# Performance work log

Hardware: AMD Instinct MI355X
Metric: run time of the kernel (lower is better)

## Reference

```python
import jax, jax.numpy as jnp
import numpy as np
from jax.scipy.linalg import expm

N_LEAVES = 8   # n
S = 64         # alphabet size (codons)
M = 8          # number of mixture model components (prod(model_shape))
N_SITES = 100000
N_NODES = 15   # n leaves + k=7 internal nodes, root = node 14


def _build_tree():
    # T[child, parent] = branch length; balanced binary tree, children < parent
    T = np.zeros((N_NODES, N_NODES), dtype=np.float32)
    parent = [8, 8, 9, 9, 10, 10, 11, 11, 12, 12, 13, 13, 14, 14]
    for c, p in enumerate(parent):
        T[c, p] = 0.05 * (1 + (c % 4))
    return T

TREE = _build_tree()


def _inv_stereographic_projection(y):
    ns = jnp.sum(y * y, axis=-1, keepdims=True)          # (M, 1)
    return jnp.concatenate([2 * y, ns - 1], axis=-1) / (ns + 1)  # (M, s)


def _build_Q(rates, pi_inv):
    r = rates ** 2                                        # (M, s(s-1)/2), nonneg
    pi = _inv_stereographic_projection(pi_inv) ** 2       # (M, s) stable probs
    iu, ju = np.triu_indices(S, 1)
    Q = jnp.zeros((M, S, S), r.dtype).at[:, iu, ju].set(r)
    Q = Q + jnp.swapaxes(Q, 1, 2)                         # symmetrize (zero diag)
    Q = Q * pi[:, None, :]
    diag = -jnp.sum(Q, axis=2)                            # (M, s)
    Q = Q.at[:, jnp.arange(S), jnp.arange(S)].set(diag)
    emut = -jnp.sum(pi * diag, axis=1)                    # expected mutations
    Q = Q / emut[:, None, None]                           # one expected mutation
    return Q, pi


def _forward(X, rates, pi_inv):
    Q, pi = _build_Q(rates, pi_inv)
    es, et = np.nonzero(TREE)                             # static edge list
    n = N_LEAVES
    k = TREE.shape[-1] - n
    t = jnp.asarray(TREE[es, et])                         # (E,) branch lengths
    # all per-edge, per-component transition matrices: expm(t * Q)
    P = jax.vmap(expm)((t[:, None, None, None] * Q[None]).reshape(-1, S, S))
    P = P.reshape(len(es), M, S, S)                       # (E, M, s, s)
    A = []  # messages at internal nodes, each (i, M, s)
    for a in range(n, n + k):
        edge_ids = np.nonzero(et == a)[0]
        msgs = []
        for ei in edge_ids:
            b = int(es[ei])
            Pab = P[ei]                                   # (M, s, s)
            if b < n:
                msgs.append(jnp.einsum('mcd,id->imc', Pab, X[:, b, :]))
            else:
                msgs.append(jnp.einsum('mcd,imd->imc', Pab, A[b - n]))
        Aa = msgs[0]
        for mmsg in msgs[1:]:
            Aa = Aa * mmsg                                # Felsenstein product
        A.append(Aa)
    # marginalize root states against stationary distribution
    return jnp.einsum('imc,mc->im', A[-1], pi)            # (i, M)


def setup_inputs() -> dict:
    key = jax.random.key(0)
    k1, k2, k3 = jax.random.split(key, 3)
    X = jax.random.uniform(k1, (N_SITES, N_LEAVES, S), dtype=jnp.float32)
    rates = jax.random.uniform(k2, (M, S * (S - 1) // 2), dtype=jnp.float32)
    pi_inv = jax.random.uniform(k3, (M, S - 1), dtype=jnp.float32)
    return {'X': X, 'rates': rates, 'pi_inv': pi_inv}


def reference(X, rates, pi_inv):
    return _forward(X, rates, pi_inv)
```

## Files before the change

### kernel.cpp

```cpp
#include <hip/hip_runtime.h>

#define NS 100000

typedef _Float16 half8v __attribute__((ext_vector_type(8)));
typedef _Float16 half4v __attribute__((ext_vector_type(4)));
typedef _Float16 half2v __attribute__((ext_vector_type(2)));
typedef float    f32x16 __attribute__((ext_vector_type(16)));
typedef unsigned int uint2v __attribute__((ext_vector_type(2)));

__device__ __forceinline__ float wave_sum64(float v) {
#pragma unroll
  for (int off = 32; off > 0; off >>= 1) v += __shfl_xor(v, off, 64);
  return v;
}
__device__ __forceinline__ float wave_max64(float v) {
#pragma unroll
  for (int off = 32; off > 0; off >>= 1) v = fmaxf(v, __shfl_xor(v, off, 64));
  return v;
}

__device__ __forceinline__ void mm64(const float* __restrict__ Lt,
                                     const float* __restrict__ Rn,
                                     int ro, int co, float r[16]) {
#pragma unroll 4
  for (int kk0 = 0; kk0 < 64; kk0 += 4) {
    float4 tv[4], av[4];
#pragma unroll
    for (int j = 0; j < 4; ++j) {
      tv[j] = *(const float4*)(Lt + (kk0 + j) * 64 + ro);
      av[j] = *(const float4*)(Rn + (kk0 + j) * 64 + co);
    }
#pragma unroll
    for (int j = 0; j < 4; ++j) {
      const float* tp = (const float*)&tv[j];
      const float* ap = (const float*)&av[j];
#pragma unroll
      for (int i = 0; i < 4; ++i)
#pragma unroll
        for (int c = 0; c < 4; ++c) r[i * 4 + c] += tp[i] * ap[c];
    }
  }
}

__global__ __launch_bounds__(256) void prep_P(const float* __restrict__ rates,
                                              const float* __restrict__ pi_inv,
                                              _Float16* __restrict__ Pw) {
  __shared__ __align__(16) float Ab[4096];
  __shared__ __align__(16) float Tt[4096];
  __shared__ __align__(16) float Sb[4096];
  __shared__ float pi_l[64];
  __shared__ float sc_sh[2];
  const int t = threadIdx.x;
  const int m = blockIdx.x;

  if (t < 64) {
    float y = (t < 63) ? pi_inv[m * 63 + t] : 0.f;
    float ns = wave_sum64(y * y);
    float ps = (t < 63) ? (2.f * y / (ns + 1.f)) : ((ns - 1.f) / (ns + 1.f));
    pi_l[t] = ps * ps;
  }
  __syncthreads();

  for (int it = 0; it < 16; ++it) {
    int e = t + 256 * it, i = e >> 6, j = e & 63;
    float v = 0.f;
    if (i != j) {
      int ii = i < j ? i : j, jj = i < j ? j : i;
      int tri = ii * 63 - (ii * (ii - 1)) / 2 + (jj - ii - 1);
      float r = rates[m * 2016 + tri];
      v = r * r * pi_l[j];
    }
    Ab[e] = v;
  }
  __syncthreads();
  if (t < 64) {
    float s = 0.f;
    for (int j = 0; j < 64; ++j) s += Ab[t * 64 + ((j + t) & 63)];
    Ab[t * 64 + t] = -s;
    float em = wave_sum64(pi_l[t] * s);
    if (t == 0) sc_sh[0] = 0.05f / em;
  }
  __syncthreads();
  const float sc0 = sc_sh[0];
  if (t < 64) {
    float s = 0.f;
    for (int i = 0; i < 64; ++i) s += fabsf(Ab[i * 64 + t]);
    float n1 = wave_max64(s * fabsf(sc0));
    if (t == 0) {
      int sq = 0;
      while (n1 > 0.25f && sq < 24) { n1 *= 0.5f; ++sq; }
      sc_sh[0] = ldexpf(sc0, -sq);
      sc_sh[1] = (float)sq;
    }
  }
  __syncthreads();
  const float scl = sc_sh[0];
  const int   sq  = (int)sc_sh[1];
  for (int it = 0; it < 16; ++it) {
    int e = t + 256 * it, i = e >> 6, j = e & 63;
    float a = Ab[e] * scl;
    Ab[e] = a;
    Tt[j * 64 + i] = a;
  }
  __syncthreads();

  const int ro = (t >> 4) * 4, co = (t & 15) * 4;
  float ss[16];
#pragma unroll
  for (int i = 0; i < 16; ++i) ss[i] = 0.f;

  for (int k = 2; k <= 8; ++k) {
    float r[16];
#pragma unroll
    for (int i = 0; i < 16; ++i) r[i] = 0.f;
    mm64(Tt, Ab, ro, co, r);
    __syncthreads();
    float inv = 1.f / (float)k;
#pragma unroll
    for (int i = 0; i < 16; ++i) { r[i] *= inv; ss[i] += r[i]; }
#pragma unroll
    for (int j = 0; j < 4; ++j) {
      float4 w = {r[0 * 4 + j], r[1 * 4 + j], r[2 * 4 + j], r[3 * 4 + j]};
      *(float4*)(Tt + (co + j) * 64 + ro) = w;
    }
    __syncthreads();
  }

  float s[16];
#pragma unroll
  for (int i = 0; i < 4; ++i)
#pragma unroll
    for (int j = 0; j < 4; ++j)
      s[i * 4 + j] = ss[i * 4 + j] + Ab[(ro + i) * 64 + co + j] +
                     (((ro + i) == (co + j)) ? 1.f : 0.f);
  __syncthreads();
#pragma unroll
  for (int i = 0; i < 4; ++i) {
    float4 w = {s[i * 4 + 0], s[i * 4 + 1], s[i * 4 + 2], s[i * 4 + 3]};
    *(float4*)(Sb + (ro + i) * 64 + co) = w;
  }
#pragma unroll
  for (int j = 0; j < 4; ++j) {
    float4 w = {s[0 * 4 + j], s[1 * 4 + j], s[2 * 4 + j], s[3 * 4 + j]};
    *(float4*)(Tt + (co + j) * 64 + ro) = w;
  }
  __syncthreads();

  for (int q = 0; q < sq; ++q) {
    float r[16];
#pragma unroll
    for (int i = 0; i < 16; ++i) r[i] = 0.f;
    mm64(Tt, Sb, ro, co, r);
    __syncthreads();
#pragma unroll
    for (int i = 0; i < 16; ++i) s[i] = r[i];
#pragma unroll
    for (int i = 0; i < 4; ++i) {
      float4 w = {s[i * 4 + 0], s[i * 4 + 1], s[i * 4 + 2], s[i * 4 + 3]};
      *(float4*)(Sb + (ro + i) * 64 + co) = w;
    }
#pragma unroll
    for (int j = 0; j < 4; ++j) {
      float4 w = {s[0 * 4 + j], s[1 * 4 + j], s[2 * 4 + j], s[3 * 4 + j]};
      *(float4*)(Tt + (co + j) * 64 + ro) = w;
    }
    __syncthreads();
  }

  _Float16* base = Pw + (size_t)m * 5 * 4096;
#pragma unroll
  for (int i = 0; i < 4; ++i) {
    half4v h1, h4;
#pragma unroll
    for (int j = 0; j < 4; ++j) {
      float v = s[i * 4 + j];
      h1[j] = (_Float16)v;
      h4[j] = (_Float16)(pi_l[ro + i] * v);
    }
    *(half4v*)(base + (ro + i) * 64 + co)            = h1;
    *(half4v*)(base + 4 * 4096 + (ro + i) * 64 + co) = h4;
  }
  float p2[16];
#pragma unroll
  for (int i = 0; i < 16; ++i) p2[i] = 0.f;
  mm64(Tt, Sb, ro, co, p2);
  __syncthreads();
#pragma unroll
  for (int i = 0; i < 4; ++i) {
    float4 w = {p2[i * 4 + 0], p2[i * 4 + 1], p2[i * 4 + 2], p2[i * 4 + 3]};
    *(float4*)(Ab + (ro + i) * 64 + co) = w;
    half4v h;
#pragma unroll
    for (int j = 0; j < 4; ++j) h[j] = (_Float16)p2[i * 4 + j];
    *(half4v*)(base + 1 * 4096 + (ro + i) * 64 + co) = h;
  }
#pragma unroll
  for (int j = 0; j < 4; ++j) {
    float4 w = {p2[0 * 4 + j], p2[1 * 4 + j], p2[2 * 4 + j], p2[3 * 4 + j]};
    *(float4*)(Tt + (co + j) * 64 + ro) = w;
  }
  __syncthreads();
  {
    float r3[16], r4[16];
#pragma unroll
    for (int i = 0; i < 16; ++i) { r3[i] = 0.f; r4[i] = 0.f; }
#pragma unroll 2
    for (int kk0 = 0; kk0 < 64; kk0 += 4) {
      float4 tv[4], a3[4], a4[4];
#pragma unroll
      for (int j = 0; j < 4; ++j) {
        tv[j] = *(const float4*)(Tt + (kk0 + j) * 64 + ro);
        a3[j] = *(const float4*)(Sb + (kk0 + j) * 64 + co);
        a4[j] = *(const float4*)(Ab + (kk0 + j) * 64 + co);
      }
#pragma unroll
      for (int j = 0; j < 4; ++j) {
        const float* tp = (const float*)&tv[j];
        const float* p3 = (const float*)&a3[j];
        const float* p4 = (const float*)&a4[j];
#pragma unroll
        for (int i = 0; i < 4; ++i)
#pragma unroll
          for (int c = 0; c < 4; ++c) {
            r3[i * 4 + c] += tp[i] * p3[c];
            r4[i * 4 + c] += tp[i] * p4[c];
          }
      }
    }
#pragma unroll
    for (int i = 0; i < 4; ++i) {
      half4v h3, h4;
#pragma unroll
      for (int j = 0; j < 4; ++j) {
        h3[j] = (_Float16)r3[i * 4 + j];
        h4[j] = (_Float16)r4[i * 4 + j];
      }
      *(half4v*)(base + 2 * 4096 + (ro + i) * 64 + co) = h3;
      *(half4v*)(base + 3 * 4096 + (ro + i) * 64 + co) = h4;
    }
  }
}

struct Pk { half2v h[16]; };
struct PF { half8v f0[4], f1[4]; };

__device__ __forceinline__ void swap32(unsigned& a, unsigned& b) {
#if __has_builtin(__builtin_amdgcn_permlane32_swap)
  uint2v r = __builtin_amdgcn_permlane32_swap(a, b, false, false);
  a = r.x; b = r.y;
#else
  unsigned pa = (unsigned)__shfl_xor((int)a, 32, 64);
  unsigned pb = (unsigned)__shfl_xor((int)b, 32, 64);
  bool hi = (threadIdx.x & 32) != 0;
  unsigned na = hi ? pb : a;
  unsigned nb = hi ? b : pa;
  a = na; b = nb;
#endif
}

__device__ __forceinline__ half8v bfrag_state(const Pk& s, int kt) {
  const int rt = kt >> 1, b = (kt & 1) * 4;
  unsigned a0 = __builtin_bit_cast(unsigned, s.h[rt * 8 + b + 0]);
  unsigned c0 = __builtin_bit_cast(unsigned, s.h[rt * 8 + b + 2]);
  unsigned a1 = __builtin_bit_cast(unsigned, s.h[rt * 8 + b + 1]);
  unsigned c1 = __builtin_bit_cast(unsigned, s.h[rt * 8 + b + 3]);
  swap32(a0, c0);
  swap32(a1, c1);
  union { half8v v; unsigned u[4]; } U;
  U.u[0] = a0; U.u[1] = a1; U.u[2] = c0; U.u[3] = c1;
  return U.v;
}

__device__ __forceinline__ void zero16(f32x16& a) {
#pragma unroll
  for (int i = 0; i < 16; ++i) a[i] = 0.f;
}

__device__ __forceinline__ Pk pack_acc(const f32x16& a0, const f32x16& a1) {
  Pk o;
#pragma unroll
  for (int p = 0; p < 8; ++p) {
    o.h[p]     = __builtin_bit_cast(half2v,
                   __builtin_amdgcn_cvt_pkrtz(a0[2 * p], a0[2 * p + 1]));
    o.h[8 + p] = __builtin_bit_cast(half2v,
                   __builtin_amdgcn_cvt_pkrtz(a1[2 * p], a1[2 * p + 1]));
  }
  return o;
}

__device__ __forceinline__ PF load_pf(const _Float16* __restrict__ Pv,
                                      int s31, int hb) {
  PF pf;
#pragma unroll
  for (int kt = 0; kt < 4; ++kt) {
    pf.f0[kt] = *(const half8v*)(Pv + (s31 * 64 + kt * 16 + hb * 8));
    pf.f1[kt] = *(const half8v*)(Pv + ((32 + s31) * 64 + kt * 16 + hb * 8));
  }
  return pf;
}

__device__ __forceinline__ Pk msg_leaf_pk(const _Float16* __restrict__ Pv,
                                          const _Float16* __restrict__ xs,
                                          int leaf, int s31, int hb, int sw) {
  PF pf = load_pf(Pv, s31, hb);
  f32x16 a0, a1;
  zero16(a0); zero16(a1);
#pragma unroll
  for (int kt = 0; kt < 4; ++kt) {
    half8v bf = *(const half8v*)(xs + s31 * 512 +
                                 ((leaf * 64 + kt * 16 + hb * 8) ^ sw));
    a0 = __builtin_amdgcn_mfma_f32_32x32x16_f16(pf.f0[kt], bf, a0, 0, 0, 0);
    a1 = __builtin_amdgcn_mfma_f32_32x32x16_f16(pf.f1[kt], bf, a1, 0, 0, 0);
  }
  return pack_acc(a0, a1);
}

__device__ __forceinline__ Pk msg_state_pk(const _Float16* __restrict__ Pv,
                                           const Pk& src, int s31, int hb) {
  PF pf = load_pf(Pv, s31, hb);
  f32x16 a0, a1;
  zero16(a0); zero16(a1);
#pragma unroll
  for (int kt = 0; kt < 4; ++kt) {
    half8v bf = bfrag_state(src, kt);
    a0 = __builtin_amdgcn_mfma_f32_32x32x16_f16(pf.f0[kt], bf, a0, 0, 0, 0);
    a1 = __builtin_amdgcn_mfma_f32_32x32x16_f16(pf.f1[kt], bf, a1, 0, 0, 0);
  }
  return pack_acc(a0, a1);
}

__device__ __forceinline__ Pk mulpk(const Pk& a, const Pk& b) {
  Pk o;
#pragma unroll
  for (int i = 0; i < 16; ++i) o.h[i] = a.h[i] * b.h[i];
  return o;
}

__global__ __launch_bounds__(256, 2) void tree_fwd(const float* __restrict__ X,
                                                   const _Float16* __restrict__ Pw,
                                                   float* __restrict__ out) {
  __shared__ __align__(16) _Float16 xs[32 * 512];
  const int t = threadIdx.x;
  const int sb0 = blockIdx.x * 32;

  for (int it = 0; it < 16; ++it) {
    int e0 = (t + 256 * it) * 4;
    int site = e0 >> 9;
    int k = e0 & 511;
    float4 v = ((const float4*)X)[(size_t)(sb0 + site) * 128 + (k >> 2)];
    half4v h;
    h.x = (_Float16)v.x; h.y = (_Float16)v.y; h.z = (_Float16)v.z; h.w = (_Float16)v.w;
    *(half4v*)(xs + site * 512 + (k ^ ((site & 7) << 3))) = h;
  }
  __syncthreads();

  const int lane = t & 63, wav = t >> 6;
  const int s31 = lane & 31, hb = lane >> 5;
  const int sw = (s31 & 7) << 3;

#pragma unroll 1
  for (int mp = 0; mp < 2; ++mp) {
    const int m = wav + 4 * mp;
    const _Float16* Pm = Pw + (size_t)m * 5 * 4096;

    Pk sA = mulpk(msg_leaf_pk(Pm + 0 * 4096, xs, 0, s31, hb, sw),
                  msg_leaf_pk(Pm + 1 * 4096, xs, 1, s31, hb, sw));
    Pk sB = mulpk(msg_leaf_pk(Pm + 2 * 4096, xs, 2, s31, hb, sw),
                  msg_leaf_pk(Pm + 3 * 4096, xs, 3, s31, hb, sw));
    Pk s12 = mulpk(msg_state_pk(Pm + 0 * 4096, sA, s31, hb),
                   msg_state_pk(Pm + 1 * 4096, sB, s31, hb));
    sA = mulpk(msg_leaf_pk(Pm + 0 * 4096, xs, 4, s31, hb, sw),
               msg_leaf_pk(Pm + 1 * 4096, xs, 5, s31, hb, sw));
    sB = mulpk(msg_leaf_pk(Pm + 2 * 4096, xs, 6, s31, hb, sw),
               msg_leaf_pk(Pm + 3 * 4096, xs, 7, s31, hb, sw));
    Pk s13 = mulpk(msg_state_pk(Pm + 2 * 4096, sA, s31, hb),
                   msg_state_pk(Pm + 3 * 4096, sB, s31, hb));
    Pk mL = msg_state_pk(Pm + 4 * 4096, s12, s31, hb);
    {
      PF pf = load_pf(Pm + 1 * 4096, s31, hb);
      f32x16 a0, a1;
      zero16(a0); zero16(a1);
#pragma unroll
      for (int kt = 0; kt < 4; ++kt) {
        half8v bf = bfrag_state(s13, kt);
        a0 = __builtin_amdgcn_mfma_f32_32x32x16_f16(pf.f0[kt], bf, a0, 0, 0, 0);
        a1 = __builtin_amdgcn_mfma_f32_32x32x16_f16(pf.f1[kt], bf, a1, 0, 0, 0);
      }
      float part = 0.f;
#pragma unroll
      for (int p = 0; p < 8; ++p) {
        part += (float)mL.h[p].x     * a0[2 * p]
              + (float)mL.h[p].y     * a0[2 * p + 1]
              + (float)mL.h[8 + p].x * a1[2 * p]
              + (float)mL.h[8 + p].y * a1[2 * p + 1];
      }
      part += __shfl_xor(part, 32, 64);
      if (lane < 32) out[(size_t)(sb0 + s31) * 8 + m] = part;
    }
  }
}

extern "C" void kernel_launch(void* const* d_in, const int* in_sizes, int n_in,
                              void* d_out, int out_size, void* d_ws, size_t ws_size,
                              hipStream_t stream) {
  const float* X      = (const float*)d_in[0];
  const float* rates  = (const float*)d_in[1];
  const float* pi_inv = (const float*)d_in[2];
  _Float16* Pw = (_Float16*)d_ws;

  prep_P<<<8, 256, 0, stream>>>(rates, pi_inv, Pw);
  tree_fwd<<<NS / 32, 256, 0, stream>>>(X, Pw, (float*)d_out);
}
```

Before: 523.9 us.

## Use 64-site blocks, split waves by site group and component, reuse P fragments

Each block now handles 64 sites instead of 32. The four waves are split into two site groups, and each wave covers four mixture components instead of two. Leaf messages are computed in pairs that share one loaded set of P fragments, and the accumulators are processed one 32-row half at a time, which lowers register pressure and the number of global loads of P. The Taylor series in prep_P is cut from 8 terms to 6, which trades expm accuracy for less setup work. LDS use doubles to 64 KB per block, which may limit occupancy, and a bounds guard is added for the partial last block.

Result: slower. 567.4 us (+8.3%).

```diff
diff --git a/kernel.cpp b/kernel.cpp
--- a/kernel.cpp
+++ b/kernel.cpp
@@ -109,7 +109,7 @@
 #pragma unroll
   for (int i = 0; i < 16; ++i) ss[i] = 0.f;
 
-  for (int k = 2; k <= 8; ++k) {
+  for (int k = 2; k <= 6; ++k) {
     float r[16];
 #pragma unroll
     for (int i = 0; i < 16; ++i) r[i] = 0.f;
@@ -242,7 +242,6 @@
 }
 
 struct Pk { half2v h[16]; };
-struct PF { half8v f0[4], f1[4]; };
 
 __device__ __forceinline__ void swap32(unsigned& a, unsigned& b) {
 #if __has_builtin(__builtin_amdgcn_permlane32_swap)
@@ -276,57 +275,90 @@
   for (int i = 0; i < 16; ++i) a[i] = 0.f;
 }
 
-__device__ __forceinline__ Pk pack_acc(const f32x16& a0, const f32x16& a1) {
+__device__ __forceinline__ half2v pk2(float x, float y) {
+  half2v h; h.x = (_Float16)x; h.y = (_Float16)y; return h;
+}
+
+__device__ __forceinline__ half8v ld_bf(const _Float16* __restrict__ xg,
+                                        int leaf, int kt, int s31, int hb, int sw) {
+  return *(const half8v*)(xg + s31 * 512 + ((leaf * 64 + kt * 16 + hb * 8) ^ sw));
+}
+
+template <bool MUL>
+__device__ __forceinline__ void leaf_pair(const _Float16* __restrict__ Pv,
+                                          const _Float16* __restrict__ xg,
+                                          int la, int lb, int s31, int hb, int sw,
+                                          Pk& A, Pk& B) {
+#pragma unroll
+  for (int hh = 0; hh < 2; ++hh) {
+    half8v pf[4];
+#pragma unroll
+    for (int kt = 0; kt < 4; ++kt)
+      pf[kt] = *(const half8v*)(Pv + ((hh * 32 + s31) * 64 + kt * 16 + hb * 8));
+    {
+      f32x16 a; zero16(a);
+#pragma unroll
+      for (int kt = 0; kt < 4; ++kt)
+        a = __builtin_amdgcn_mfma_f32_32x32x16_f16(pf[kt], ld_bf(xg, la, kt, s31, hb, sw), a, 0, 0, 0);
+#pragma unroll
+      for (int p = 0; p < 8; ++p) {
+        half2v v = pk2(a[2 * p], a[2 * p + 1]);
+        A.h[hh * 8 + p] = MUL ? (half2v)(A.h[hh * 8 + p] * v) : v;
+      }
+    }
+    {
+      f32x16 b; zero16(b);
+#pragma unroll
+      for (int kt = 0; kt < 4; ++kt)
+        b = __builtin_amdgcn_mfma_f32_32x32x16_f16(pf[kt], ld_bf(xg, lb, kt, s31, hb, sw), b, 0, 0, 0);
+#pragma unroll
+      for (int p = 0; p < 8; ++p) {
+        half2v v = pk2(b[2 * p], b[2 * p + 1]);
+        B.h[hh * 8 + p] = MUL ? (half2v)(B.h[hh * 8 + p] * v) : v;
+      }
+    }
+  }
+}
+
+__device__ __forceinline__ Pk state_msg(const _Float16* __restrict__ Pv,
+                                        const Pk& src, int s31, int hb) {
   Pk o;
 #pragma unroll
-  for (int p = 0; p < 8; ++p) {
-    o.h[p]     = __builtin_bit_cast(half2v,
-                   __builtin_amdgcn_cvt_pkrtz(a0[2 * p], a0[2 * p + 1]));
-    o.h[8 + p] = __builtin_bit_cast(half2v,
-                   __builtin_amdgcn_cvt_pkrtz(a1[2 * p], a1[2 * p + 1]));
+  for (int hh = 0; hh < 2; ++hh) {
+    half8v pf[4];
+#pragma unroll
+    for (int kt = 0; kt < 4; ++kt)
+      pf[kt] = *(const half8v*)(Pv + ((hh * 32 + s31) * 64 + kt * 16 + hb * 8));
+    f32x16 a; zero16(a);
+#pragma unroll
+    for (int kt = 0; kt < 4; ++kt)
+      a = __builtin_amdgcn_mfma_f32_32x32x16_f16(pf[kt], bfrag_state(src, kt), a, 0, 0, 0);
+#pragma unroll
+    for (int p = 0; p < 8; ++p) o.h[hh * 8 + p] = pk2(a[2 * p], a[2 * p + 1]);
   }
   return o;
 }
 
-__device__ __forceinline__ PF load_pf(const _Float16* __restrict__ Pv,
-                                      int s31, int hb) {
-  PF pf;
-#pragma unroll
-  for (int kt = 0; kt < 4; ++kt) {
-    pf.f0[kt] = *(const half8v*)(Pv + (s31 * 64 + kt * 16 + hb * 8));
-    pf.f1[kt] = *(const half8v*)(Pv + ((32 + s31) * 64 + kt * 16 + hb * 8));
-  }
-  return pf;
-}
-
-__device__ __forceinline__ Pk msg_leaf_pk(const _Float16* __restrict__ Pv,
-                                          const _Float16* __restrict__ xs,
-                                          int leaf, int s31, int hb, int sw) {
-  PF pf = load_pf(Pv, s31, hb);
-  f32x16 a0, a1;
-  zero16(a0); zero16(a1);
-#pragma unroll
-  for (int kt = 0; kt < 4; ++kt) {
-    half8v bf = *(const half8v*)(xs + s31 * 512 +
-                                 ((leaf * 64 + kt * 16 + hb * 8) ^ sw));
-    a0 = __builtin_amdgcn_mfma_f32_32x32x16_f16(pf.f0[kt], bf, a0, 0, 0, 0);
-    a1 = __builtin_amdgcn_mfma_f32_32x32x16_f16(pf.f1[kt], bf, a1, 0, 0, 0);
-  }
-  return pack_acc(a0, a1);
-}
-
-__device__ __forceinline__ Pk msg_state_pk(const _Float16* __restrict__ Pv,
-                                           const Pk& src, int s31, int hb) {
-  PF pf = load_pf(Pv, s31, hb);
-  f32x16 a0, a1;
-  zero16(a0); zero16(a1);
-#pragma unroll
-  for (int kt = 0; kt < 4; ++kt) {
-    half8v bf = bfrag_state(src, kt);
-    a0 = __builtin_amdgcn_mfma_f32_32x32x16_f16(pf.f0[kt], bf, a0, 0, 0, 0);
-    a1 = __builtin_amdgcn_mfma_f32_32x32x16_f16(pf.f1[kt], bf, a1, 0, 0, 0);
-  }
-  return pack_acc(a0, a1);
+__device__ __forceinline__ float root_dot(const _Float16* __restrict__ Pv,
+                                          const Pk& s13, const Pk& m12,
+                                          int s31, int hb) {
+  float part = 0.f;
+#pragma unroll
+  for (int hh = 0; hh < 2; ++hh) {
+    half8v pf[4];
+#pragma unroll
+    for (int kt = 0; kt < 4; ++kt)
+      pf[kt] = *(const half8v*)(Pv + ((hh * 32 + s31) * 64 + kt * 16 + hb * 8));
+    f32x16 a; zero16(a);
+#pragma unroll
+    for (int kt = 0; kt < 4; ++kt)
+      a = __builtin_amdgcn_mfma_f32_32x32x16_f16(pf[kt], bfrag_state(s13, kt), a, 0, 0, 0);
+#pragma unroll
+    for (int p = 0; p < 8; ++p)
+      part += (float)m12.h[hh * 8 + p].x * a[2 * p]
+            + (float)m12.h[hh * 8 + p].y * a[2 * p + 1];
+  }
+  return part;
 }
 
 __device__ __forceinline__ Pk mulpk(const Pk& a, const Pk& b) {
@@ -339,15 +371,17 @@
 __global__ __launch_bounds__(256, 2) void tree_fwd(const float* __restrict__ X,
                                                    const _Float16* __restrict__ Pw,
                                                    float* __restrict__ out) {
-  __shared__ __align__(16) _Float16 xs[32 * 512];
+  __shared__ __align__(16) _Float16 xs[64 * 512];
   const int t = threadIdx.x;
-  const int sb0 = blockIdx.x * 32;
-
-  for (int it = 0; it < 16; ++it) {
+  const int sb0 = blockIdx.x * 64;
+  const int nsv = (NS - sb0) < 64 ? (NS - sb0) : 64;
+
+  for (int it = 0; it < 32; ++it) {
     int e0 = (t + 256 * it) * 4;
     int site = e0 >> 9;
     int k = e0 & 511;
-    float4 v = ((const float4*)X)[(size_t)(sb0 + site) * 128 + (k >> 2)];
+    float4 v = {0.f, 0.f, 0.f, 0.f};
+    if (site < nsv) v = ((const float4*)X)[(size_t)(sb0 + site) * 128 + (k >> 2)];
     half4v h;
     h.x = (_Float16)v.x; h.y = (_Float16)v.y; h.z = (_Float16)v.z; h.w = (_Float16)v.w;
     *(half4v*)(xs + site * 512 + (k ^ ((site & 7) << 3))) = h;
@@ -357,46 +391,34 @@
   const int lane = t & 63, wav = t >> 6;
   const int s31 = lane & 31, hb = lane >> 5;
   const int sw = (s31 & 7) << 3;
+  const int grp = wav >> 1;
+  const int mbase = (wav & 1) * 4;
+  const _Float16* xg = xs + grp * 32 * 512;
+  const int siteG = sb0 + grp * 32 + s31;
 
 #pragma unroll 1
-  for (int mp = 0; mp < 2; ++mp) {
-    const int m = wav + 4 * mp;
+  for (int mi = 0; mi < 4; ++mi) {
+    const int m = mbase + mi;
     const _Float16* Pm = Pw + (size_t)m * 5 * 4096;
-
-    Pk sA = mulpk(msg_leaf_pk(Pm + 0 * 4096, xs, 0, s31, hb, sw),
-                  msg_leaf_pk(Pm + 1 * 4096, xs, 1, s31, hb, sw));
-    Pk sB = mulpk(msg_leaf_pk(Pm + 2 * 4096, xs, 2, s31, hb, sw),
-                  msg_leaf_pk(Pm + 3 * 4096, xs, 3, s31, hb, sw));
-    Pk s12 = mulpk(msg_state_pk(Pm + 0 * 4096, sA, s31, hb),
-                   msg_state_pk(Pm + 1 * 4096, sB, s31, hb));
-    sA = mulpk(msg_leaf_pk(Pm + 0 * 4096, xs, 4, s31, hb, sw),
-               msg_leaf_pk(Pm + 1 * 4096, xs, 5, s31, hb, sw));
-    sB = mulpk(msg_leaf_pk(Pm + 2 * 4096, xs, 6, s31, hb, sw),
-               msg_leaf_pk(Pm + 3 * 4096, xs, 7, s31, hb, sw));
-    Pk s13 = mulpk(msg_state_pk(Pm + 2 * 4096, sA, s31, hb),
-                   msg_state_pk(Pm + 3 * 4096, sB, s31, hb));
-    Pk mL = msg_state_pk(Pm + 4 * 4096, s12, s31, hb);
-    {
-      PF pf = load_pf(Pm + 1 * 4096, s31, hb);
-      f32x16 a0, a1;
-      zero16(a0); zero16(a1);
-#pragma unroll
-      for (int kt = 0; kt < 4; ++kt) {
-        half8v bf = bfrag_state(s13, kt);
-        a0 = __builtin_amdgcn_mfma_f32_32x32x16_f16(pf.f0[kt], bf, a0, 0, 0, 0);
-        a1 = __builtin_amdgcn_mfma_f32_32x32x16_f16(pf.f1[kt], bf, a1, 0, 0, 0);
-      }
-      float part = 0.f;
-#pragma unroll
-      for (int p = 0; p < 8; ++p) {
-        part += (float)mL.h[p].x     * a0[2 * p]
-              + (float)mL.h[p].y     * a0[2 * p + 1]
-              + (float)mL.h[8 + p].x * a1[2 * p]
-              + (float)mL.h[8 + p].y * a1[2 * p + 1];
-      }
-      part += __shfl_xor(part, 32, 64);
-      if (lane < 32) out[(size_t)(sb0 + s31) * 8 + m] = part;
-    }
+    const _Float16* v0 = Pm;
+    const _Float16* v1 = Pm + 4096;
+    const _Float16* v2 = Pm + 2 * 4096;
+    const _Float16* v3 = Pm + 3 * 4096;
+    const _Float16* v4 = Pm + 4 * 4096;
+
+    Pk A, B, C, D;
+    leaf_pair<false>(v0, xg, 0, 4, s31, hb, sw, A, B);
+    leaf_pair<true >(v1, xg, 1, 5, s31, hb, sw, A, B);
+    leaf_pair<false>(v2, xg, 2, 6, s31, hb, sw, C, D);
+    leaf_pair<true >(v3, xg, 3, 7, s31, hb, sw, C, D);
+    Pk m8  = state_msg(v0, A, s31, hb);
+    Pk s12 = mulpk(m8, state_msg(v1, C, s31, hb));
+    Pk m10 = state_msg(v2, B, s31, hb);
+    Pk s13 = mulpk(m10, state_msg(v3, D, s31, hb));
+    Pk m12 = state_msg(v4, s12, s31, hb);
+    float part = root_dot(v1, s13, m12, s31, hb);
+    part += __shfl_xor(part, 32, 64);
+    if (lane < 32 && siteG < NS) out[(size_t)siteG * 8 + m] = part;
   }
 }
 
@@ -409,5 +431,5 @@
   _Float16* Pw = (_Float16*)d_ws;
 
   prep_P<<<8, 256, 0, stream>>>(rates, pi_inv, Pw);
-  tree_fwd<<<NS / 32, 256, 0, stream>>>(X, Pw, (float*)d_out);
-}
+  tree_fwd<<<(NS + 63) / 64, 256, 0, stream>>>(X, Pw, (float*)d_out);
+}
```
